# Kernel optimization log

Measured on AMD Instinct MI355X. Metric: run time of the kernel, lower is better.

The kernel has to match this reference:

```python
import jax, jax.numpy as jnp
import numpy as np

N = 50000          # num nodes
E = 800000         # num edges
H, C = 2, 64       # heads, per-head channels (hidden_dim=64)
IN_DIM = 128
EDGE_DIM = 32
NEG_SLOPE = 0.2


def setup_inputs() -> dict:
    key = jax.random.key(0)
    ks = jax.random.split(key, 20)
    s = 0.05
    inp = {
        'x': jax.random.normal(ks[0], (N, IN_DIM), jnp.float32),
        'edge_index': jax.random.randint(ks[1], (2, E), 0, N, jnp.int64),
        'edge_attr': jax.random.normal(ks[2], (E, EDGE_DIM), jnp.float32),
    }
    k = 3
    for l in range(3):
        inp[f'Wl{l}'] = jax.random.normal(ks[k], (IN_DIM, H * C), jnp.float32) * s; k += 1
        inp[f'Wr{l}'] = jax.random.normal(ks[k], (IN_DIM, H * C), jnp.float32) * s; k += 1
        inp[f'We{l}'] = jax.random.normal(ks[k], (EDGE_DIM, H * C), jnp.float32) * s; k += 1
        inp[f'att{l}'] = jax.random.normal(ks[k], (H, C), jnp.float32) * s; k += 1
        inp[f'b{l}'] = jnp.zeros((H * C,), jnp.float32)
    return inp


def gatv2_layer(x, src, dst, edge_attr, Wl, Wr, We, att, b):
    # PyG GATv2Conv (concat=True, share_weights=False):
    #   e_ij = att . LeakyReLU(Wl x_j + Wr x_i + We edge_ij)
    #   alpha = softmax_j over neighborhood of dst i; out_i = sum_j alpha_ij * (Wl x_j)
    xl = (x @ Wl).reshape(-1, H, C)              # [N,H,C] source transform
    xr = (x @ Wr).reshape(-1, H, C)              # [N,H,C] target transform
    ea = (edge_attr @ We).reshape(-1, H, C)      # [E,H,C]
    xj = xl[src]                                 # [E,H,C] gather source
    e = jax.nn.leaky_relu(xj + xr[dst] + ea, NEG_SLOPE)
    logits = jnp.einsum('ehc,hc->eh', e, att)    # [E,H]
    # segment softmax over dst neighborhoods
    m = jax.ops.segment_max(logits, dst, num_segments=N)  # [N,H]
    m = jnp.where(jnp.isfinite(m), m, 0.0)
    ex = jnp.exp(logits - m[dst])
    denom = jax.ops.segment_sum(ex, dst, num_segments=N)  # [N,H]
    alpha = ex / (denom[dst] + 1e-16)            # [E,H]
    out = jax.ops.segment_sum(alpha[:, :, None] * xj, dst, num_segments=N)  # [N,H,C]
    return out.reshape(-1, H * C) + b


def reference(x, edge_index, edge_attr,
              Wl0, Wr0, We0, att0, b0,
              Wl1, Wr1, We1, att1, b1,
              Wl2, Wr2, We2, att2, b2):
    src, dst = edge_index[0], edge_index[1]
    h = gatv2_layer(x, src, dst, edge_attr, Wl0, Wr0, We0, att0, b0)
    h = jax.nn.relu(h)
    h = gatv2_layer(h, src, dst, edge_attr, Wl1, Wr1, We1, att1, b1)
    h = jax.nn.relu(h)
    h = gatv2_layer(h, src, dst, edge_attr, Wl2, Wr2, We2, att2, b2)
    return h
```

## Files before the change

kernel.cpp:

```cpp
#include <hip/hip_runtime.h>

typedef unsigned int u32;
typedef unsigned short u16;
typedef __attribute__((ext_vector_type(8))) short bf16x8;
typedef __attribute__((ext_vector_type(4))) float f32x4;

__device__ __forceinline__ u16 f2b(float f){
  u32 x = __float_as_uint(f);
  u32 r = (x + 0x7fffu + ((x >> 16) & 1u)) >> 16;
  return (u16)r;
}
__device__ __forceinline__ float b2f(u16 h){ return __uint_as_float((u32)h << 16); }
__device__ __forceinline__ float bl(u32 u){ return __uint_as_float(u << 16); }
__device__ __forceinline__ float bh(u32 u){ return __uint_as_float(u & 0xffff0000u); }


__global__ void k_detect(const u32* __restrict__ ei, int n, u32* __restrict__ flag){
  int t = blockIdx.x * blockDim.x + threadIdx.x;
  u32 v = 0;
  if (t < n) v = ei[2 * t + 1];
  unsigned long long b = __ballot(v != 0u);
  if ((threadIdx.x & 63) == 0 && b) atomicOr(flag, 1u);
}

__global__ void k_convhist(const int* __restrict__ ei, int* __restrict__ src, int* __restrict__ dst,
                           int* __restrict__ deg, const float* __restrict__ eattr,
                           u16* __restrict__ ea2, int E, const u32* __restrict__ flag){
  int e = blockIdx.x * blockDim.x + threadIdx.x;
  if (e >= E) return;
  bool is64 = (*flag == 0u);
  int s, d;
  if (is64){ s = ei[2 * e]; d = ei[2 * (E + e)]; }
  else     { s = ei[e];     d = ei[E + e]; }
  src[e] = s; dst[e] = d;
  atomicAdd(&deg[d], 1);
  const float4* srow = (const float4*)(eattr + (size_t)e * 32);
  u32 pk[16];
  #pragma unroll
  for (int i = 0; i < 8; i++){
    float4 v = srow[i];
    pk[2*i]   = (u32)f2b(v.x) | ((u32)f2b(v.y) << 16);
    pk[2*i+1] = (u32)f2b(v.z) | ((u32)f2b(v.w) << 16);
  }
  uint4* drow = (uint4*)(ea2 + (size_t)e * 32);
  drow[0] = make_uint4(pk[0], pk[1], pk[2], pk[3]);
  drow[1] = make_uint4(pk[4], pk[5], pk[6], pk[7]);
  drow[2] = make_uint4(pk[8], pk[9], pk[10], pk[11]);
  drow[3] = make_uint4(pk[12], pk[13], pk[14], pk[15]);
}

__global__ __launch_bounds__(256) void k_scan1(const int* __restrict__ deg, int* __restrict__ bsum, int n,
                                               int* __restrict__ ssrc, int* __restrict__ sdst,
                                               u16* __restrict__ ea2s_pad, int E){
  int b = blockIdx.x, t = threadIdx.x, lane = t & 63, wv = t >> 6;
  if (b == 0){
    if (t < 64){ ssrc[E + t] = 0; sdst[E + t] = 0; }
    ((uint4*)ea2s_pad)[t] = make_uint4(0, 0, 0, 0);
  }
  int i0 = b * 1024 + t * 4;
  int4 v = make_int4(0,0,0,0);
  if (i0 + 3 < n) v = *(const int4*)(deg + i0);
  else { if (i0 < n) v.x = deg[i0]; if (i0+1 < n) v.y = deg[i0+1]; if (i0+2 < n) v.z = deg[i0+2]; }
  int s = v.x + v.y + v.z + v.w;
  #pragma unroll
  for (int off = 1; off < 64; off <<= 1) s += __shfl_xor(s, off);
  __shared__ int ws[4];
  if (lane == 0) ws[wv] = s;
  __syncthreads();
  if (t == 0) bsum[b] = ws[0] + ws[1] + ws[2] + ws[3];
}

__global__ __launch_bounds__(1024) void k_scan2(int* __restrict__ bsum, int nb, int* __restrict__ segN){
  int t = threadIdx.x, lane = t & 63, w = t >> 6;
  int v = (t < nb) ? bsum[t] : 0;
  int x = v;
  #pragma unroll
  for (int off = 1; off < 64; off <<= 1){
    int y = __shfl_up(x, off);
    if (lane >= off) x += y;
  }
  __shared__ int wsum[16];
  if (lane == 63) wsum[w] = x;
  __syncthreads();
  if (w == 0 && lane < 16){
    int sv = wsum[lane];
    #pragma unroll
    for (int off = 1; off < 16; off <<= 1){
      int y = __shfl_up(sv, off);
      if (lane >= off) sv += y;
    }
    wsum[lane] = sv;
  }
  __syncthreads();
  int woff = (w > 0) ? wsum[w - 1] : 0;
  if (t < nb) bsum[t] = woff + x - v;
  if (t == 0) *segN = wsum[15];
}

__global__ __launch_bounds__(256) void k_scan3(const int* __restrict__ deg, const int* __restrict__ bsum,
                                               int* __restrict__ seg, int n){
  int b = blockIdx.x, t = threadIdx.x, lane = t & 63, wv = t >> 6;
  int i0 = b * 1024 + t * 4;
  int4 v = make_int4(0,0,0,0);
  if (i0 + 3 < n) v = *(const int4*)(deg + i0);
  else { if (i0 < n) v.x = deg[i0]; if (i0+1 < n) v.y = deg[i0+1]; if (i0+2 < n) v.z = deg[i0+2]; }
  int s = v.x + v.y + v.z + v.w;
  int x = s;
  #pragma unroll
  for (int off = 1; off < 64; off <<= 1){
    int y = __shfl_up(x, off);
    if (lane >= off) x += y;
  }
  __shared__ int ws[4];
  if (lane == 63) ws[wv] = x;
  __syncthreads();
  int woff = 0;
  #pragma unroll
  for (int k = 0; k < 4; k++) if (k < wv) woff += ws[k];
  int base = bsum[b] + woff + (x - s);
  if (i0 < n)     seg[i0]     = base;
  if (i0+1 < n)   seg[i0+1]   = base + v.x;
  if (i0+2 < n)   seg[i0+2]   = base + v.x + v.y;
  if (i0+3 < n)   seg[i0+3]   = base + v.x + v.y + v.z;
}

__global__ void k_scatter(const int* __restrict__ src, const int* __restrict__ dst,
                          const int* __restrict__ seg, int* __restrict__ cur,
                          int* __restrict__ ssrc, int* __restrict__ sdst,
                          int* __restrict__ seid, int E){
  int e = blockIdx.x * blockDim.x + threadIdx.x;
  if (e >= E) return;
  int d = dst[e];
  int pos = seg[d] + atomicAdd(&cur[d], 1);
  ssrc[pos] = src[e];
  sdst[pos] = d;
  seid[pos] = e;
}

__global__ void k_sortb(const int* __restrict__ seid, const u16* __restrict__ ea2o,
                        u16* __restrict__ ea2s, int E){
  int t = blockIdx.x * blockDim.x + threadIdx.x;
  int e = t >> 2, j = t & 3;
  if (e >= E) return;
  int eid = seid[e];
  uint4 v = *(const uint4*)(ea2o + (size_t)eid * 32 + j * 8);
  *(uint4*)(ea2s + (size_t)e * 32 + j * 8) = v;
}

__global__ __launch_bounds__(256) void k_prepw(
    const float* __restrict__ W0, const float* __restrict__ W1, const float* __restrict__ W2,
    const float* __restrict__ W3, const float* __restrict__ W4, const float* __restrict__ W5,
    u16* __restrict__ WtH, u16* __restrict__ WtL)
{
  int mat = blockIdx.z;
  const float* W = (mat == 0) ? W0 : (mat == 1) ? W1 : (mat == 2) ? W2 :
                   (mat == 3) ? W3 : (mat == 4) ? W4 : W5;
  __shared__ float tile[32][33];
  int kt = blockIdx.x * 32, ct = blockIdx.y * 32;
  int tr = threadIdx.x & 31, ti = threadIdx.x >> 5;
  #pragma unroll
  for (int j = 0; j < 4; j++){
    int kk = ti + 8 * j;
    tile[kk][tr] = W[(size_t)(kt + kk) * 128 + ct + tr];
  }
  __syncthreads();
  #pragma unroll
  for (int j = 0; j < 4; j++){
    int cc = ti + 8 * j;
    float v = tile[tr][cc];
    u16 hi = f2b(v);
    u16 lo = f2b(v - b2f(hi));
    size_t o = (size_t)mat * 16384 + (size_t)(ct + cc) * 128 + kt + tr;
    WtH[o] = hi;
    WtL[o] = lo;
  }
}

__global__ __launch_bounds__(256) void k_gemm2(
    const float* __restrict__ A,
    const u16* __restrict__ WtH, const u16* __restrict__ WtL,
    u16* __restrict__ xlb, u16* __restrict__ xrb, int nrows)
{
  __shared__ u16 sAH[64][72], sAL[64][72];
  __shared__ u16 sWH[128][72], sWL[128][72];
  int t = threadIdx.x, wv = t >> 6, lane = t & 63;
  int col = lane & 15, kg = lane >> 4;
  int r0 = blockIdx.x * 64;
  int mat = blockIdx.y;
  const u16* WHb = WtH + (size_t)mat * 16384;
  const u16* WLb = WtL + (size_t)mat * 16384;

  f32x4 acc[4][2];
  #pragma unroll
  for (int m = 0; m < 4; m++)
    #pragma unroll
    for (int n = 0; n < 2; n++)
      acc[m][n] = (f32x4){0.f, 0.f, 0.f, 0.f};

  int ar = t >> 2, ak = (t & 3) << 4;
  int wc = t >> 1, wk = (t & 1) << 5;

  for (int kh = 0; kh < 2; kh++){
    __syncthreads();
    {
      int gr = r0 + ar;
      const float* ap = A + (size_t)gr * 128 + kh * 64 + ak;
      float4 va = {0,0,0,0}, vb = {0,0,0,0}, vc = {0,0,0,0}, vd = {0,0,0,0};
      if (gr < nrows){
        va = *(const float4*)ap; vb = *(const float4*)(ap + 4);
        vc = *(const float4*)(ap + 8); vd = *(const float4*)(ap + 12);
      }
      float fv[16] = { va.x, va.y, va.z, va.w, vb.x, vb.y, vb.z, vb.w,
                       vc.x, vc.y, vc.z, vc.w, vd.x, vd.y, vd.z, vd.w };
      u32 hp[8], lp[8];
      #pragma unroll
      for (int i = 0; i < 8; i++){
        u16 h0 = f2b(fv[2*i]),   h1 = f2b(fv[2*i+1]);
        u16 l0 = f2b(fv[2*i]   - b2f(h0));
        u16 l1 = f2b(fv[2*i+1] - b2f(h1));
        hp[i] = (u32)h0 | ((u32)h1 << 16);
        lp[i] = (u32)l0 | ((u32)l1 << 16);
      }
      *(uint4*)&sAH[ar][ak]     = make_uint4(hp[0], hp[1], hp[2], hp[3]);
      *(uint4*)&sAH[ar][ak + 8] = make_uint4(hp[4], hp[5], hp[6], hp[7]);
      *(uint4*)&sAL[ar][ak]     = make_uint4(lp[0], lp[1], lp[2], lp[3]);
      *(uint4*)&sAL[ar][ak + 8] = make_uint4(lp[4], lp[5], lp[6], lp[7]);
    }
    {
      const u16* gh = WHb + (size_t)wc * 128 + kh * 64 + wk;
      const u16* gl = WLb + (size_t)wc * 128 + kh * 64 + wk;
      uint4 h0 = *(const uint4*)gh, h1 = *(const uint4*)(gh + 8);
      uint4 h2 = *(const uint4*)(gh + 16), h3 = *(const uint4*)(gh + 24);
      uint4 l0 = *(const uint4*)gl, l1 = *(const uint4*)(gl + 8);
      uint4 l2 = *(const uint4*)(gl + 16), l3 = *(const uint4*)(gl + 24);
      *(uint4*)&sWH[wc][wk]      = h0; *(uint4*)&sWH[wc][wk + 8]  = h1;
      *(uint4*)&sWH[wc][wk + 16] = h2; *(uint4*)&sWH[wc][wk + 24] = h3;
      *(uint4*)&sWL[wc][wk]      = l0; *(uint4*)&sWL[wc][wk + 8]  = l1;
      *(uint4*)&sWL[wc][wk + 16] = l2; *(uint4*)&sWL[wc][wk + 24] = l3;
    }
    __syncthreads();
    #pragma unroll
    for (int ks = 0; ks < 2; ks++){
      bf16x8 bhi0 = *(const bf16x8*)&sWH[wv*32 + col]     [ks*32 + kg*8];
      bf16x8 bhi1 = *(const bf16x8*)&sWH[wv*32 + 16 + col][ks*32 + kg*8];
      bf16x8 blo0 = *(const bf16x8*)&sWL[wv*32 + col]     [ks*32 + kg*8];
      bf16x8 blo1 = *(const bf16x8*)&sWL[wv*32 + 16 + col][ks*32 + kg*8];
      #pragma unroll
      for (int m = 0; m < 4; m++){
        bf16x8 ahv = *(const bf16x8*)&sAH[m*16 + col][ks*32 + kg*8];
        bf16x8 alv = *(const bf16x8*)&sAL[m*16 + col][ks*32 + kg*8];
        acc[m][0] = __builtin_amdgcn_mfma_f32_16x16x32_bf16(ahv, bhi0, acc[m][0], 0, 0, 0);
        acc[m][0] = __builtin_amdgcn_mfma_f32_16x16x32_bf16(alv, bhi0, acc[m][0], 0, 0, 0);
        acc[m][0] = __builtin_amdgcn_mfma_f32_16x16x32_bf16(ahv, blo0, acc[m][0], 0, 0, 0);
        acc[m][1] = __builtin_amdgcn_mfma_f32_16x16x32_bf16(ahv, bhi1, acc[m][1], 0, 0, 0);
        acc[m][1] = __builtin_amdgcn_mfma_f32_16x16x32_bf16(alv, bhi1, acc[m][1], 0, 0, 0);
        acc[m][1] = __builtin_amdgcn_mfma_f32_16x16x32_bf16(ahv, blo1, acc[m][1], 0, 0, 0);
      }
    }
  }
  u16* ob = mat ? xrb : xlb;
  #pragma unroll
  for (int m = 0; m < 4; m++){
    #pragma unroll
    for (int n = 0; n < 2; n++){
      #pragma unroll
      for (int r = 0; r < 4; r++){
        int row = r0 + m*16 + kg*4 + r;
        int c   = wv*32 + n*16 + col;
        if (row < nrows) ob[(size_t)row * 128 + c] = f2b(acc[m][n][r]);
      }
    }
  }
}

__global__ __launch_bounds__(256) void k_edge(
    const int* __restrict__ ssrc, const int* __restrict__ sdst,
    const u16* __restrict__ ea2s,
    const u16* __restrict__ xlb, const u16* __restrict__ xrb,
    const float* __restrict__ We, const float* __restrict__ att,
    float2* __restrict__ pr2, int ntiles, int E)
{
  __shared__ float sD[4][16][132];
  int wv = threadIdx.x >> 6, lane = threadIdx.x & 63;
  int col = lane & 15, kg = lane >> 4;
  int er = lane >> 2, q = lane & 3;

  bf16x8 bw[8];
  #pragma unroll
  for (int c = 0; c < 8; c++)
    #pragma unroll
    for (int j = 0; j < 8; j++)
      bw[c][j] = (short)f2b(We[(kg * 8 + j) * 128 + c * 16 + col]);
  u32 attp[16];
  #pragma unroll
  for (int i = 0; i < 16; i++)
    attp[i] = (u32)f2b(att[q * 32 + 2*i]) | ((u32)f2b(att[q * 32 + 2*i + 1]) << 16);

  int nw = gridDim.x * 4;
  int t = blockIdx.x * 4 + wv;
  if (t >= ntiles) return;

  int e0 = t * 16;
  bf16x8 a = *(const bf16x8*)(ea2s + (size_t)(e0 + col) * 32 + kg * 8);
  int p = e0 + er;
  int sn = ssrc[p], dn = sdst[p];
  const u16* xjp = xlb + (size_t)sn * 128 + q * 32;
  uint4 j0 = ((const uint4*)xjp)[0], j1 = ((const uint4*)xjp)[1],
        j2 = ((const uint4*)xjp)[2], j3 = ((const uint4*)xjp)[3];

  while (true){
    const u16* xip = xrb + (size_t)dn * 128 + q * 32;
    uint4 i0 = ((const uint4*)xip)[0], i1 = ((const uint4*)xip)[1],
          i2 = ((const uint4*)xip)[2], i3 = ((const uint4*)xip)[3];

    int t2 = t + nw;
    bool more = (t2 < ntiles);
    int tc = more ? t2 : t;
    int e02 = tc * 16;
    int p2 = e02 + er;
    int sn2 = ssrc[p2], dn2 = sdst[p2];
    bf16x8 a2 = *(const bf16x8*)(ea2s + (size_t)(e02 + col) * 32 + kg * 8);
    const u16* xj2 = xlb + (size_t)sn2 * 128 + q * 32;
    uint4 nj0 = ((const uint4*)xj2)[0], nj1 = ((const uint4*)xj2)[1],
          nj2 = ((const uint4*)xj2)[2], nj3 = ((const uint4*)xj2)[3];

    #pragma unroll
    for (int c = 0; c < 8; c++){
      f32x4 d = __builtin_amdgcn_mfma_f32_16x16x32_bf16(a, bw[c], (f32x4){0.f,0.f,0.f,0.f}, 0, 0, 0);
      #pragma unroll
      for (int r = 0; r < 4; r++)
        sD[wv][kg * 4 + r][c * 16 + col] = d[r];
    }

    const float* drow = &sD[wv][er][q * 32];
    float acc = 0.f;
#define EPK(KO, JQ, IQ) { \
    float4 d0 = *(const float4*)(drow + KO*8); \
    float4 d1 = *(const float4*)(drow + KO*8 + 4); \
    float v; u32 jw, iw, aw; \
    jw = JQ.x; iw = IQ.x; aw = attp[KO*4+0]; \
    v = d0.x + bl(jw) + bl(iw); v = fmaxf(v, 0.2f*v); acc = fmaf(v, bl(aw), acc); \
    v = d0.y + bh(jw) + bh(iw); v = fmaxf(v, 0.2f*v); acc = fmaf(v, bh(aw), acc); \
    jw = JQ.y; iw = IQ.y; aw = attp[KO*4+1]; \
    v = d0.z + bl(jw) + bl(iw); v = fmaxf(v, 0.2f*v); acc = fmaf(v, bl(aw), acc); \
    v = d0.w + bh(jw) + bh(iw); v = fmaxf(v, 0.2f*v); acc = fmaf(v, bh(aw), acc); \
    jw = JQ.z; iw = IQ.z; aw = attp[KO*4+2]; \
    v = d1.x + bl(jw) + bl(iw); v = fmaxf(v, 0.2f*v); acc = fmaf(v, bl(aw), acc); \
    v = d1.y + bh(jw) + bh(iw); v = fmaxf(v, 0.2f*v); acc = fmaf(v, bh(aw), acc); \
    jw = JQ.w; iw = IQ.w; aw = attp[KO*4+3]; \
    v = d1.z + bl(jw) + bl(iw); v = fmaxf(v, 0.2f*v); acc = fmaf(v, bl(aw), acc); \
    v = d1.w + bh(jw) + bh(iw); v = fmaxf(v, 0.2f*v); acc = fmaf(v, bh(aw), acc); }
    EPK(0, j0, i0) EPK(1, j1, i1) EPK(2, j2, i2) EPK(3, j3, i3)
#undef EPK
    acc += __shfl_xor(acc, 1);
    float other = __shfl_xor(acc, 2);
    if (q == 0 && p < E){
      pr2[p] = make_float2(__expf(fminf(acc, 80.f)), __expf(fminf(other, 80.f)));
    }
    if (!more) break;
    t = t2; p = p2; dn = dn2; a = a2;
    j0 = nj0; j1 = nj1; j2 = nj2; j3 = nj3;
  }
}

template<int RELU>
__global__ __launch_bounds__(256) void k_seg2(
    const int* __restrict__ seg, const int* __restrict__ ssrc,
    const float2* __restrict__ pr2,
    const u16* __restrict__ xlb, const float* __restrict__ bias,
    float* __restrict__ out, int N)
{
  int wid  = blockIdx.x * 4 + (threadIdx.x >> 6);
  int lane = threadIdx.x & 63;
  if (wid >= N) return;
  int eg = lane >> 4, cb = lane & 15, c0 = cb * 8;
  int hsel = cb >> 3;

  int p0 = seg[wid], p1 = seg[wid + 1];
  float s = 0.f;
  float o0 = 0.f, o1 = 0.f, o2 = 0.f, o3 = 0.f, o4 = 0.f, o5 = 0.f, o6 = 0.f, o7 = 0.f;

  if (p0 < p1){
#define LDB(PP, QV, XV) { \
    int ii = PP + eg; ii = (ii < p1) ? ii : (p1 - 1); \
    int sn = ssrc[ii]; \
    QV = pr2[ii]; \
    XV = *(const uint4*)(xlb + (size_t)sn * 128 + c0); }
    float2 qa; uint4 xa;
    LDB(p0, qa, xa)
    int p = p0;
    while (true){
      int pn = p + 4;
      bool more = pn < p1;
      int pc = more ? pn : p;
      float2 qb; uint4 xb;
      LDB(pc, qb, xb)
      float e = hsel ? qa.y : qa.x;
      if (p + eg >= p1) e = 0.f;
      s += e;
      o0 = fmaf(e, bl(xa.x), o0); o1 = fmaf(e, bh(xa.x), o1);
      o2 = fmaf(e, bl(xa.y), o2); o3 = fmaf(e, bh(xa.y), o3);
      o4 = fmaf(e, bl(xa.z), o4); o5 = fmaf(e, bh(xa.z), o5);
      o6 = fmaf(e, bl(xa.w), o6); o7 = fmaf(e, bh(xa.w), o7);
      if (!more) break;
      p = pn; qa = qb; xa = xb;
    }
#undef LDB
  }
  s  += __shfl_xor(s, 16);  s  += __shfl_xor(s, 32);
  o0 += __shfl_xor(o0, 16); o0 += __shfl_xor(o0, 32);
  o1 += __shfl_xor(o1, 16); o1 += __shfl_xor(o1, 32);
  o2 += __shfl_xor(o2, 16); o2 += __shfl_xor(o2, 32);
  o3 += __shfl_xor(o3, 16); o3 += __shfl_xor(o3, 32);
  o4 += __shfl_xor(o4, 16); o4 += __shfl_xor(o4, 32);
  o5 += __shfl_xor(o5, 16); o5 += __shfl_xor(o5, 32);
  o6 += __shfl_xor(o6, 16); o6 += __shfl_xor(o6, 32);
  o7 += __shfl_xor(o7, 16); o7 += __shfl_xor(o7, 32);

  if (eg == 0){
    float inv = 1.0f / (s + 1e-16f);
    float4 b0 = *(const float4*)(bias + c0);
    float4 b1 = *(const float4*)(bias + c0 + 4);
    float r0 = fmaf(o0, inv, b0.x), r1 = fmaf(o1, inv, b0.y);
    float r2 = fmaf(o2, inv, b0.z), r3 = fmaf(o3, inv, b0.w);
    float r4 = fmaf(o4, inv, b1.x), r5 = fmaf(o5, inv, b1.y);
    float r6 = fmaf(o6, inv, b1.z), r7 = fmaf(o7, inv, b1.w);
    if (RELU){
      r0 = fmaxf(r0, 0.f); r1 = fmaxf(r1, 0.f); r2 = fmaxf(r2, 0.f); r3 = fmaxf(r3, 0.f);
      r4 = fmaxf(r4, 0.f); r5 = fmaxf(r5, 0.f); r6 = fmaxf(r6, 0.f); r7 = fmaxf(r7, 0.f);
    }
    *(float4*)(out + (size_t)wid * 128 + c0)     = make_float4(r0, r1, r2, r3);
    *(float4*)(out + (size_t)wid * 128 + c0 + 4) = make_float4(r4, r5, r6, r7);
  }
}

extern "C" void kernel_launch(void* const* d_in, const int* in_sizes, int n_in,
                              void* d_out, int out_size, void* d_ws, size_t ws_size,
                              hipStream_t stream)
{
  const float* x     = (const float*)d_in[0];
  const int*   ei    = (const int*)  d_in[1];
  const float* eattr = (const float*)d_in[2];
  const float* Wp[3][5];
  for (int l = 0; l < 3; l++)
    for (int j = 0; j < 5; j++)
      Wp[l][j] = (const float*)d_in[3 + l * 5 + j];

  int N = in_sizes[0] / 128;
  int E = in_sizes[2] / 32;

  char* w = (char*)d_ws;
  auto alloc = [&](size_t bytes) -> char* {
    char* p = w; w += (bytes + 255) & ~(size_t)255; return p;
  };
  float* xr   = (float*)alloc((size_t)N * 128 * 4);
  u16*   xlb  = (u16*)  alloc((size_t)N * 128 * 2);
  u16*   xrb  = (u16*)  alloc((size_t)N * 128 * 2);
  u16*   ea2o = (u16*)  alloc((size_t)E * 32 * 2);
  u16*   ea2s = (u16*)  alloc((size_t)(E + 64) * 32 * 2);
  float2* prb = (float2*)alloc((size_t)E * 8);
  u16*   WtH  = (u16*)  alloc((size_t)6 * 16384 * 2);
  u16*   WtL  = (u16*)  alloc((size_t)6 * 16384 * 2);
  int* srcA   = (int*)alloc((size_t)E * 4);
  int* dstA   = (int*)alloc((size_t)E * 4);
  int* ssrc   = (int*)alloc((size_t)(E + 64) * 4);
  int* sdst   = (int*)alloc((size_t)(E + 64) * 4);
  int* seid   = (int*)alloc((size_t)E * 4);
  int* seg    = (int*)alloc((size_t)(N + 1) * 4);
  int* bsum   = (int*)alloc(1024 * 4);
  char* zbase = alloc((size_t)N * 4);      int* deg  = (int*)zbase;
  char* zcur  = alloc((size_t)N * 4);      int* cur  = (int*)zcur;
  char* zflag = alloc(256);                u32* flag = (u32*)zflag;
  size_t zspan = (size_t)(zflag + 256 - zbase);

  hipMemsetAsync(zbase, 0, zspan, stream);

  int ndet = (E < 16384) ? E : 16384;
  k_detect<<<(ndet + 255) / 256, 256, 0, stream>>>((const u32*)ei, ndet, flag);
  int gE = (E + 255) / 256;
  k_convhist<<<gE, 256, 0, stream>>>(ei, srcA, dstA, deg, eattr, ea2o, E, flag);
  int nb = (N + 1023) / 1024;
  k_scan1<<<nb, 256, 0, stream>>>(deg, bsum, N, ssrc, sdst, ea2s + (size_t)E * 32, E);
  k_scan2<<<1, 1024, 0, stream>>>(bsum, nb, seg + N);
  k_scan3<<<nb, 256, 0, stream>>>(deg, bsum, seg, N);
  k_scatter<<<gE, 256, 0, stream>>>(srcA, dstA, seg, cur, ssrc, sdst, seid, E);
  k_sortb<<<(E * 4 + 255) / 256, 256, 0, stream>>>(seid, ea2o, ea2s, E);
  dim3 gp(4, 4, 6);
  k_prepw<<<gp, 256, 0, stream>>>(Wp[0][0], Wp[0][1], Wp[1][0], Wp[1][1], Wp[2][0], Wp[2][1], WtH, WtL);

  int gS = (N + 3) / 4;
  int ntiles = (E + 15) / 16;
  int gEdge = (ntiles + 3) / 4; if (gEdge > 2048) gEdge = 2048;
  dim3 gG2((N + 63) / 64, 2);

  const float* hin = x;
  for (int l = 0; l < 3; l++){
    k_gemm2<<<gG2, 256, 0, stream>>>(hin, WtH + (size_t)l * 2 * 16384, WtL + (size_t)l * 2 * 16384, xlb, xrb, N);
    k_edge<<<gEdge, 256, 0, stream>>>(ssrc, sdst, ea2s, xlb, xrb, Wp[l][2], Wp[l][3], prb, ntiles, E);
    float* outp = (l == 2) ? (float*)d_out : xr;
    if (l == 2) k_seg2<0><<<gS, 256, 0, stream>>>(seg, ssrc, prb, xlb, Wp[l][4], outp, N);
    else        k_seg2<1><<<gS, 256, 0, stream>>>(seg, ssrc, prb, xlb, Wp[l][4], outp, N);
    hin = xr;
  }
}
```

Baseline: 489.8 us.

## Cut register and LDS pressure in edge and GEMM kernels to raise occupancy

The edge kernel now keeps the bf16 We fragments in shared memory instead of 8 register vectors. It computes the attention logit one head at a time through a half-sized LDS staging buffer, drops the cross-iteration prefetch of source rows, and requests 6 waves per SIMD via launch_bounds. The GEMM kernel switches to 32-wide K slices with smaller unpadded LDS tiles and four K iterations. The goal is higher occupancy to hide gather latency, at the cost of more syncs and LDS reads, lost prefetch overlap, and possible bank conflicts from the unpadded GEMM tiles.

```diff
diff --git a/kernel.cpp b/kernel.cpp
--- a/kernel.cpp
+++ b/kernel.cpp
@@ -181,8 +181,8 @@
     const u16* __restrict__ WtH, const u16* __restrict__ WtL,
     u16* __restrict__ xlb, u16* __restrict__ xrb, int nrows)
 {
-  __shared__ u16 sAH[64][72], sAL[64][72];
-  __shared__ u16 sWH[128][72], sWL[128][72];
+  __shared__ u16 sAH[64][32], sAL[64][32];
+  __shared__ u16 sWH[128][32], sWL[128][32];
   int t = threadIdx.x, wv = t >> 6, lane = t & 63;
   int col = lane & 15, kg = lane >> 4;
   int r0 = blockIdx.x * 64;
@@ -197,65 +197,52 @@
     for (int n = 0; n < 2; n++)
       acc[m][n] = (f32x4){0.f, 0.f, 0.f, 0.f};
 
-  int ar = t >> 2, ak = (t & 3) << 4;
-  int wc = t >> 1, wk = (t & 1) << 5;
-
-  for (int kh = 0; kh < 2; kh++){
+  int ar = t >> 2, ak = (t & 3) << 3;
+  int wc = t >> 1, wk = (t & 1) << 4;
+
+  for (int kh = 0; kh < 4; kh++){
     __syncthreads();
     {
       int gr = r0 + ar;
-      const float* ap = A + (size_t)gr * 128 + kh * 64 + ak;
-      float4 va = {0,0,0,0}, vb = {0,0,0,0}, vc = {0,0,0,0}, vd = {0,0,0,0};
-      if (gr < nrows){
-        va = *(const float4*)ap; vb = *(const float4*)(ap + 4);
-        vc = *(const float4*)(ap + 8); vd = *(const float4*)(ap + 12);
-      }
-      float fv[16] = { va.x, va.y, va.z, va.w, vb.x, vb.y, vb.z, vb.w,
-                       vc.x, vc.y, vc.z, vc.w, vd.x, vd.y, vd.z, vd.w };
-      u32 hp[8], lp[8];
+      const float* ap = A + (size_t)gr * 128 + kh * 32 + ak;
+      float4 va = {0,0,0,0}, vb = {0,0,0,0};
+      if (gr < nrows){ va = *(const float4*)ap; vb = *(const float4*)(ap + 4); }
+      float fv[8] = { va.x, va.y, va.z, va.w, vb.x, vb.y, vb.z, vb.w };
+      u32 hp[4], lp[4];
       #pragma unroll
-      for (int i = 0; i < 8; i++){
+      for (int i = 0; i < 4; i++){
         u16 h0 = f2b(fv[2*i]),   h1 = f2b(fv[2*i+1]);
         u16 l0 = f2b(fv[2*i]   - b2f(h0));
         u16 l1 = f2b(fv[2*i+1] - b2f(h1));
         hp[i] = (u32)h0 | ((u32)h1 << 16);
         lp[i] = (u32)l0 | ((u32)l1 << 16);
       }
-      *(uint4*)&sAH[ar][ak]     = make_uint4(hp[0], hp[1], hp[2], hp[3]);
-      *(uint4*)&sAH[ar][ak + 8] = make_uint4(hp[4], hp[5], hp[6], hp[7]);
-      *(uint4*)&sAL[ar][ak]     = make_uint4(lp[0], lp[1], lp[2], lp[3]);
-      *(uint4*)&sAL[ar][ak + 8] = make_uint4(lp[4], lp[5], lp[6], lp[7]);
+      *(uint4*)&sAH[ar][ak] = make_uint4(hp[0], hp[1], hp[2], hp[3]);
+      *(uint4*)&sAL[ar][ak] = make_uint4(lp[0], lp[1], lp[2], lp[3]);
     }
     {
-      const u16* gh = WHb + (size_t)wc * 128 + kh * 64 + wk;
-      const u16* gl = WLb + (size_t)wc * 128 + kh * 64 + wk;
+      const u16* gh = WHb + (size_t)wc * 128 + kh * 32 + wk;
+      const u16* gl = WLb + (size_t)wc * 128 + kh * 32 + wk;
       uint4 h0 = *(const uint4*)gh, h1 = *(const uint4*)(gh + 8);
-      uint4 h2 = *(const uint4*)(gh + 16), h3 = *(const uint4*)(gh + 24);
       uint4 l0 = *(const uint4*)gl, l1 = *(const uint4*)(gl + 8);
-      uint4 l2 = *(const uint4*)(gl + 16), l3 = *(const uint4*)(gl + 24);
-      *(uint4*)&sWH[wc][wk]      = h0; *(uint4*)&sWH[wc][wk + 8]  = h1;
-      *(uint4*)&sWH[wc][wk + 16] = h2; *(uint4*)&sWH[wc][wk + 24] = h3;
-      *(uint4*)&sWL[wc][wk]      = l0; *(uint4*)&sWL[wc][wk + 8]  = l1;
-      *(uint4*)&sWL[wc][wk + 16] = l2; *(uint4*)&sWL[wc][wk + 24] = l3;
+      *(uint4*)&sWH[wc][wk]     = h0; *(uint4*)&sWH[wc][wk + 8] = h1;
+      *(uint4*)&sWL[wc][wk]     = l0; *(uint4*)&sWL[wc][wk + 8] = l1;
     }
     __syncthreads();
-    #pragma unroll
-    for (int ks = 0; ks < 2; ks++){
-      bf16x8 bhi0 = *(const bf16x8*)&sWH[wv*32 + col]     [ks*32 + kg*8];
-      bf16x8 bhi1 = *(const bf16x8*)&sWH[wv*32 + 16 + col][ks*32 + kg*8];
-      bf16x8 blo0 = *(const bf16x8*)&sWL[wv*32 + col]     [ks*32 + kg*8];
-      bf16x8 blo1 = *(const bf16x8*)&sWL[wv*32 + 16 + col][ks*32 + kg*8];
-      #pragma unroll
-      for (int m = 0; m < 4; m++){
-        bf16x8 ahv = *(const bf16x8*)&sAH[m*16 + col][ks*32 + kg*8];
-        bf16x8 alv = *(const bf16x8*)&sAL[m*16 + col][ks*32 + kg*8];
-        acc[m][0] = __builtin_amdgcn_mfma_f32_16x16x32_bf16(ahv, bhi0, acc[m][0], 0, 0, 0);
-        acc[m][0] = __builtin_amdgcn_mfma_f32_16x16x32_bf16(alv, bhi0, acc[m][0], 0, 0, 0);
-        acc[m][0] = __builtin_amdgcn_mfma_f32_16x16x32_bf16(ahv, blo0, acc[m][0], 0, 0, 0);
-        acc[m][1] = __builtin_amdgcn_mfma_f32_16x16x32_bf16(ahv, bhi1, acc[m][1], 0, 0, 0);
-        acc[m][1] = __builtin_amdgcn_mfma_f32_16x16x32_bf16(alv, bhi1, acc[m][1], 0, 0, 0);
-        acc[m][1] = __builtin_amdgcn_mfma_f32_16x16x32_bf16(ahv, blo1, acc[m][1], 0, 0, 0);
-      }
+    bf16x8 bhi0 = *(const bf16x8*)&sWH[wv*32 + col]     [kg*8];
+    bf16x8 bhi1 = *(const bf16x8*)&sWH[wv*32 + 16 + col][kg*8];
+    bf16x8 blo0 = *(const bf16x8*)&sWL[wv*32 + col]     [kg*8];
+    bf16x8 blo1 = *(const bf16x8*)&sWL[wv*32 + 16 + col][kg*8];
+    #pragma unroll
+    for (int m = 0; m < 4; m++){
+      bf16x8 ahv = *(const bf16x8*)&sAH[m*16 + col][kg*8];
+      bf16x8 alv = *(const bf16x8*)&sAL[m*16 + col][kg*8];
+      acc[m][0] = __builtin_amdgcn_mfma_f32_16x16x32_bf16(ahv, bhi0, acc[m][0], 0, 0, 0);
+      acc[m][0] = __builtin_amdgcn_mfma_f32_16x16x32_bf16(alv, bhi0, acc[m][0], 0, 0, 0);
+      acc[m][0] = __builtin_amdgcn_mfma_f32_16x16x32_bf16(ahv, blo0, acc[m][0], 0, 0, 0);
+      acc[m][1] = __builtin_amdgcn_mfma_f32_16x16x32_bf16(ahv, bhi1, acc[m][1], 0, 0, 0);
+      acc[m][1] = __builtin_amdgcn_mfma_f32_16x16x32_bf16(alv, bhi1, acc[m][1], 0, 0, 0);
+      acc[m][1] = __builtin_amdgcn_mfma_f32_16x16x32_bf16(ahv, blo1, acc[m][1], 0, 0, 0);
     }
   }
   u16* ob = mat ? xrb : xlb;
@@ -273,28 +260,37 @@
   }
 }
 
-__global__ __launch_bounds__(256) void k_edge(
+__global__ __launch_bounds__(256, 6) void k_edge(
     const int* __restrict__ ssrc, const int* __restrict__ sdst,
     const u16* __restrict__ ea2s,
     const u16* __restrict__ xlb, const u16* __restrict__ xrb,
     const float* __restrict__ We, const float* __restrict__ att,
     float2* __restrict__ pr2, int ntiles, int E)
 {
-  __shared__ float sD[4][16][132];
-  int wv = threadIdx.x >> 6, lane = threadIdx.x & 63;
+  __shared__ u16  sBW[8][64][8];
+  __shared__ float sDh[4][16][68];
+  int tid = threadIdx.x;
+  for (int s = tid; s < 512; s += 256){
+    int c = s >> 6, ln = s & 63;
+    int kgq = ln >> 4, colq = ln & 15;
+    #pragma unroll
+    for (int j = 0; j < 8; j++)
+      sBW[c][ln][j] = f2b(We[(kgq * 8 + j) * 128 + c * 16 + colq]);
+  }
+  __syncthreads();
+
+  int wv = tid >> 6, lane = tid & 63;
   int col = lane & 15, kg = lane >> 4;
   int er = lane >> 2, q = lane & 3;
 
-  bf16x8 bw[8];
-  #pragma unroll
-  for (int c = 0; c < 8; c++)
-    #pragma unroll
-    for (int j = 0; j < 8; j++)
-      bw[c][j] = (short)f2b(We[(kg * 8 + j) * 128 + c * 16 + col]);
   u32 attp[16];
   #pragma unroll
-  for (int i = 0; i < 16; i++)
-    attp[i] = (u32)f2b(att[q * 32 + 2*i]) | ((u32)f2b(att[q * 32 + 2*i + 1]) << 16);
+  for (int h = 0; h < 2; h++)
+    #pragma unroll
+    for (int i = 0; i < 8; i++){
+      int ch = h * 64 + q * 16 + 2 * i;
+      attp[h * 8 + i] = (u32)f2b(att[ch]) | ((u32)f2b(att[ch + 1]) << 16);
+    }
 
   int nw = gridDim.x * 4;
   int t = blockIdx.x * 4 + wv;
@@ -304,14 +300,14 @@
   bf16x8 a = *(const bf16x8*)(ea2s + (size_t)(e0 + col) * 32 + kg * 8);
   int p = e0 + er;
   int sn = ssrc[p], dn = sdst[p];
-  const u16* xjp = xlb + (size_t)sn * 128 + q * 32;
-  uint4 j0 = ((const uint4*)xjp)[0], j1 = ((const uint4*)xjp)[1],
-        j2 = ((const uint4*)xjp)[2], j3 = ((const uint4*)xjp)[3];
 
   while (true){
-    const u16* xip = xrb + (size_t)dn * 128 + q * 32;
-    uint4 i0 = ((const uint4*)xip)[0], i1 = ((const uint4*)xip)[1],
-          i2 = ((const uint4*)xip)[2], i3 = ((const uint4*)xip)[3];
+    const u16* xjr = xlb + (size_t)sn * 128;
+    const u16* xir = xrb + (size_t)dn * 128;
+    uint4 ja0 = *(const uint4*)(xjr + q * 16);
+    uint4 ja1 = *(const uint4*)(xjr + q * 16 + 8);
+    uint4 ia0 = *(const uint4*)(xir + q * 16);
+    uint4 ia1 = *(const uint4*)(xir + q * 16 + 8);
 
     int t2 = t + nw;
     bool more = (t2 < ntiles);
@@ -320,46 +316,99 @@
     int p2 = e02 + er;
     int sn2 = ssrc[p2], dn2 = sdst[p2];
     bf16x8 a2 = *(const bf16x8*)(ea2s + (size_t)(e02 + col) * 32 + kg * 8);
-    const u16* xj2 = xlb + (size_t)sn2 * 128 + q * 32;
-    uint4 nj0 = ((const uint4*)xj2)[0], nj1 = ((const uint4*)xj2)[1],
-          nj2 = ((const uint4*)xj2)[2], nj3 = ((const uint4*)xj2)[3];
-
-    #pragma unroll
-    for (int c = 0; c < 8; c++){
-      f32x4 d = __builtin_amdgcn_mfma_f32_16x16x32_bf16(a, bw[c], (f32x4){0.f,0.f,0.f,0.f}, 0, 0, 0);
+
+    #pragma unroll
+    for (int c = 0; c < 4; c++){
+      bf16x8 bwc = *(const bf16x8*)&sBW[c][lane][0];
+      f32x4 d = __builtin_amdgcn_mfma_f32_16x16x32_bf16(a, bwc, (f32x4){0.f,0.f,0.f,0.f}, 0, 0, 0);
       #pragma unroll
       for (int r = 0; r < 4; r++)
-        sD[wv][kg * 4 + r][c * 16 + col] = d[r];
-    }
-
-    const float* drow = &sD[wv][er][q * 32];
-    float acc = 0.f;
-#define EPK(KO, JQ, IQ) { \
-    float4 d0 = *(const float4*)(drow + KO*8); \
-    float4 d1 = *(const float4*)(drow + KO*8 + 4); \
-    float v; u32 jw, iw, aw; \
-    jw = JQ.x; iw = IQ.x; aw = attp[KO*4+0]; \
-    v = d0.x + bl(jw) + bl(iw); v = fmaxf(v, 0.2f*v); acc = fmaf(v, bl(aw), acc); \
-    v = d0.y + bh(jw) + bh(iw); v = fmaxf(v, 0.2f*v); acc = fmaf(v, bh(aw), acc); \
-    jw = JQ.y; iw = IQ.y; aw = attp[KO*4+1]; \
-    v = d0.z + bl(jw) + bl(iw); v = fmaxf(v, 0.2f*v); acc = fmaf(v, bl(aw), acc); \
-    v = d0.w + bh(jw) + bh(iw); v = fmaxf(v, 0.2f*v); acc = fmaf(v, bh(aw), acc); \
-    jw = JQ.z; iw = IQ.z; aw = attp[KO*4+2]; \
-    v = d1.x + bl(jw) + bl(iw); v = fmaxf(v, 0.2f*v); acc = fmaf(v, bl(aw), acc); \
-    v = d1.y + bh(jw) + bh(iw); v = fmaxf(v, 0.2f*v); acc = fmaf(v, bh(aw), acc); \
-    jw = JQ.w; iw = IQ.w; aw = attp[KO*4+3]; \
-    v = d1.z + bl(jw) + bl(iw); v = fmaxf(v, 0.2f*v); acc = fmaf(v, bl(aw), acc); \
-    v = d1.w + bh(jw) + bh(iw); v = fmaxf(v, 0.2f*v); acc = fmaf(v, bh(aw), acc); }
-    EPK(0, j0, i0) EPK(1, j1, i1) EPK(2, j2, i2) EPK(3, j3, i3)
-#undef EPK
-    acc += __shfl_xor(acc, 1);
-    float other = __shfl_xor(acc, 2);
+        sDh[wv][kg * 4 + r][c * 16 + col] = d[r];
+    }
+
+    uint4 jb0 = *(const uint4*)(xjr + 64 + q * 16);
+    uint4 jb1 = *(const uint4*)(xjr + 64 + q * 16 + 8);
+    uint4 ib0 = *(const uint4*)(xir + 64 + q * 16);
+    uint4 ib1 = *(const uint4*)(xir + 64 + q * 16 + 8);
+
+    const float* dr = &sDh[wv][er][q * 16];
+
+#define EPH(D0, D1, JW0, IW0, AW0, JW1, IW1, AW1, ACC) { \
+    float v0 = D0.x + bl(JW0) + bl(IW0); v0 = fmaxf(v0, 0.2f*v0); ACC = fmaf(v0, bl(AW0), ACC); \
+    float v1 = D0.y + bh(JW0) + bh(IW0); v1 = fmaxf(v1, 0.2f*v1); ACC = fmaf(v1, bh(AW0), ACC); \
+    float v2 = D0.z + bl(JW1) + bl(IW1); v2 = fmaxf(v2, 0.2f*v2); ACC = fmaf(v2, bl(AW1), ACC); \
+    float v3 = D0.w + bh(JW1) + bh(IW1); v3 = fmaxf(v3, 0.2f*v3); ACC = fmaf(v3, bh(AW1), ACC); \
+    (void)D1; }
+
+    float hA = 0.f;
+    {
+      float4 d0 = *(const float4*)(dr);
+      float4 d1 = *(const float4*)(dr + 4);
+      float4 d2 = *(const float4*)(dr + 8);
+      float4 d3 = *(const float4*)(dr + 12);
+      float v;
+      v = d0.x + bl(ja0.x) + bl(ia0.x); v = fmaxf(v, 0.2f*v); hA = fmaf(v, bl(attp[0]), hA);
+      v = d0.y + bh(ja0.x) + bh(ia0.x); v = fmaxf(v, 0.2f*v); hA = fmaf(v, bh(attp[0]), hA);
+      v = d0.z + bl(ja0.y) + bl(ia0.y); v = fmaxf(v, 0.2f*v); hA = fmaf(v, bl(attp[1]), hA);
+      v = d0.w + bh(ja0.y) + bh(ia0.y); v = fmaxf(v, 0.2f*v); hA = fmaf(v, bh(attp[1]), hA);
+      v = d1.x + bl(ja0.z) + bl(ia0.z); v = fmaxf(v, 0.2f*v); hA = fmaf(v, bl(attp[2]), hA);
+      v = d1.y + bh(ja0.z) + bh(ia0.z); v = fmaxf(v, 0.2f*v); hA = fmaf(v, bh(attp[2]), hA);
+      v = d1.z + bl(ja0.w) + bl(ia0.w); v = fmaxf(v, 0.2f*v); hA = fmaf(v, bl(attp[3]), hA);
+      v = d1.w + bh(ja0.w) + bh(ia0.w); v = fmaxf(v, 0.2f*v); hA = fmaf(v, bh(attp[3]), hA);
+      v = d2.x + bl(ja1.x) + bl(ia1.x); v = fmaxf(v, 0.2f*v); hA = fmaf(v, bl(attp[4]), hA);
+      v = d2.y + bh(ja1.x) + bh(ia1.x); v = fmaxf(v, 0.2f*v); hA = fmaf(v, bh(attp[4]), hA);
+      v = d2.z + bl(ja1.y) + bl(ia1.y); v = fmaxf(v, 0.2f*v); hA = fmaf(v, bl(attp[5]), hA);
+      v = d2.w + bh(ja1.y) + bh(ia1.y); v = fmaxf(v, 0.2f*v); hA = fmaf(v, bh(attp[5]), hA);
+      v = d3.x + bl(ja1.z) + bl(ia1.z); v = fmaxf(v, 0.2f*v); hA = fmaf(v, bl(attp[6]), hA);
+      v = d3.y + bh(ja1.z) + bh(ia1.z); v = fmaxf(v, 0.2f*v); hA = fmaf(v, bh(attp[6]), hA);
+      v = d3.z + bl(ja1.w) + bl(ia1.w); v = fmaxf(v, 0.2f*v); hA = fmaf(v, bl(attp[7]), hA);
+      v = d3.w + bh(ja1.w) + bh(ia1.w); v = fmaxf(v, 0.2f*v); hA = fmaf(v, bh(attp[7]), hA);
+    }
+    hA += __shfl_xor(hA, 1);
+    hA += __shfl_xor(hA, 2);
+
+    #pragma unroll
+    for (int c = 4; c < 8; c++){
+      bf16x8 bwc = *(const bf16x8*)&sBW[c][lane][0];
+      f32x4 d = __builtin_amdgcn_mfma_f32_16x16x32_bf16(a, bwc, (f32x4){0.f,0.f,0.f,0.f}, 0, 0, 0);
+      #pragma unroll
+      for (int r = 0; r < 4; r++)
+        sDh[wv][kg * 4 + r][(c - 4) * 16 + col] = d[r];
+    }
+
+    float hB = 0.f;
+    {
+      float4 d0 = *(const float4*)(dr);
+      float4 d1 = *(const float4*)(dr + 4);
+      float4 d2 = *(const float4*)(dr + 8);
+      float4 d3 = *(const float4*)(dr + 12);
+      float v;
+      v = d0.x + bl(jb0.x) + bl(ib0.x); v = fmaxf(v, 0.2f*v); hB = fmaf(v, bl(attp[8]), hB);
+      v = d0.y + bh(jb0.x) + bh(ib0.x); v = fmaxf(v, 0.2f*v); hB = fmaf(v, bh(attp[8]), hB);
+      v = d0.z + bl(jb0.y) + bl(ib0.y); v = fmaxf(v, 0.2f*v); hB = fmaf(v, bl(attp[9]), hB);
+      v = d0.w + bh(jb0.y) + bh(ib0.y); v = fmaxf(v, 0.2f*v); hB = fmaf(v, bh(attp[9]), hB);
+      v = d1.x + bl(jb0.z) + bl(ib0.z); v = fmaxf(v, 0.2f*v); hB = fmaf(v, bl(attp[10]), hB);
+      v = d1.y + bh(jb0.z) + bh(ib0.z); v = fmaxf(v, 0.2f*v); hB = fmaf(v, bh(attp[10]), hB);
+      v = d1.z + bl(jb0.w) + bl(ib0.w); v = fmaxf(v, 0.2f*v); hB = fmaf(v, bl(attp[11]), hB);
+      v = d1.w + bh(jb0.w) + bh(ib0.w); v = fmaxf(v, 0.2f*v); hB = fmaf(v, bh(attp[11]), hB);
+      v = d2.x + bl(jb1.x) + bl(ib1.x); v = fmaxf(v, 0.2f*v); hB = fmaf(v, bl(attp[12]), hB);
+      v = d2.y + bh(jb1.x) + bh(ib1.x); v = fmaxf(v, 0.2f*v); hB = fmaf(v, bh(attp[12]), hB);
+      v = d2.z + bl(jb1.y) + bl(ib1.y); v = fmaxf(v, 0.2f*v); hB = fmaf(v, bl(attp[13]), hB);
+      v = d2.w + bh(jb1.y) + bh(ib1.y); v = fmaxf(v, 0.2f*v); hB = fmaf(v, bh(attp[13]), hB);
+      v = d3.x + bl(jb1.z) + bl(ib1.z); v = fmaxf(v, 0.2f*v); hB = fmaf(v, bl(attp[14]), hB);
+      v = d3.y + bh(jb1.z) + bh(ib1.z); v = fmaxf(v, 0.2f*v); hB = fmaf(v, bh(attp[14]), hB);
+      v = d3.z + bl(jb1.w) + bl(ib1.w); v = fmaxf(v, 0.2f*v); hB = fmaf(v, bl(attp[15]), hB);
+      v = d3.w + bh(jb1.w) + bh(ib1.w); v = fmaxf(v, 0.2f*v); hB = fmaf(v, bh(attp[15]), hB);
+    }
+    hB += __shfl_xor(hB, 1);
+    hB += __shfl_xor(hB, 2);
+#undef EPH
+
     if (q == 0 && p < E){
-      pr2[p] = make_float2(__expf(fminf(acc, 80.f)), __expf(fminf(other, 80.f)));
+      pr2[p] = make_float2(__expf(fminf(hA, 80.f)), __expf(fminf(hB, 80.f)));
     }
     if (!more) break;
-    t = t2; p = p2; dn = dn2; a = a2;
-    j0 = nj0; j1 = nj1; j2 = nj2; j3 = nj3;
+    t = t2; p = p2; sn = sn2; dn = dn2; a = a2;
   }
 }
 
```

New measurement: 983.2 us. +100.8%, slower.
